# Performance work log

Measured on AMD Instinct MI355X. Metric: run time of the kernel, lower is better.

The kernel has to match this reference:

```python
import jax, jax.numpy as jnp
import numpy as np

N, D = 1024, 64  # n_nodes, inputSize == hiddenSize == cellSize


def setup_inputs() -> dict:
    key = jax.random.key(0)
    ks = jax.random.split(key, 9)
    inputs = jax.random.normal(ks[0], (N, D), dtype=jnp.float32)
    # sparse-ish binary adjacency, no self loops
    adj = (jax.random.uniform(ks[1], (N, N)) < 0.03).astype(jnp.float32)
    adj = adj.at[jnp.arange(N), jnp.arange(N)].set(0.0)
    numNei = jnp.maximum(adj.sum(axis=1), 1.0)  # avoid div-by-zero
    # initStates() in torch uses randn for h0/c0
    h0 = jax.random.normal(ks[2], (N, D), dtype=jnp.float32)
    c0 = jax.random.normal(ks[3], (N, D), dtype=jnp.float32)
    # torch nn.Linear default init: U(-1/sqrt(fan_in), 1/sqrt(fan_in))
    s_g = 1.0 / np.sqrt(2 * D)
    s_h = 1.0 / np.sqrt(D)
    Wg = jax.random.uniform(ks[4], (D, 2 * D), minval=-s_g, maxval=s_g, dtype=jnp.float32)
    bg = jax.random.uniform(ks[5], (D,), minval=-s_g, maxval=s_g, dtype=jnp.float32)
    Ws = jax.random.uniform(ks[6], (D, D), minval=-s_h, maxval=s_h, dtype=jnp.float32)
    bs = jax.random.uniform(ks[7], (D,), minval=-s_h, maxval=s_h, dtype=jnp.float32)
    Wn = jax.random.uniform(ks[8], (D, D), minval=-s_h, maxval=s_h, dtype=jnp.float32)
    sequence = jnp.arange(N, dtype=jnp.int32)
    return {"inputs": inputs, "neighbour": adj, "numNei": numNei,
            "h0": h0, "c0": c0, "Wg": Wg, "bg": bg, "Ws": Ws, "bs": bs,
            "Wn": Wn, "sequence": sequence}


def reference(inputs, neighbour, numNei, h0, c0, Wg, bg, Ws, bs, Wn, sequence):
    def step(carry, idx):
        H, C = carry                       # [N, D] each
        inp = inputs[idx]                  # [D]
        h_i = H[idx]                       # [D]
        c_i = C[idx]                       # [D] (torch passes cellState[index])
        nei = neighbour[idx]               # [N] adjacency row
        num = numNei[idx]
        # neighbour-averaged hidden state
        neiH = (nei @ H) / num             # [D]
        pre = jnp.concatenate([inp, h_i]) @ Wg.T + bg + neiH @ Wn.T  # [D]
        inputState = jax.nn.sigmoid(pre)
        outputState = inputState           # identical expression in torch
        helpCell = jnp.tanh(pre)
        fs = inp @ Ws.T + bs               # selfGate(inp), [D]
        # forgetSelfMat broadcast of fs over all nodes
        neiForget = jax.nn.sigmoid(fs[None, :] + H @ Wn.T)   # [N, D]
        forgetState = jax.nn.sigmoid(fs + h_i @ Wn.T)        # [D]
        c_new = (nei @ (neiForget * c_i[None, :])) / num \
                + forgetState * c_i + inputState * helpCell  # [D]
        h_new = jnp.tanh(outputState * c_new)
        return (H.at[idx].set(h_new), C.at[idx].set(c_new)), None

    (Hf, _Cf), _ = jax.lax.scan(step, (h0, c0), sequence)
    # torch: residualHidden aliases hiddenState and is mutated in-place,
    # so `hiddenState + residualHidden` == 2 * final hidden state.
    return Hf + Hf
```

## Files before the change

### kernel.cpp

```cpp
#include <hip/hip_runtime.h>

#define NN 1024
#define DD 64
#define CAP 96
#define RCAP 128
#define SENT 32768
#define NL2E -1.44269504088896f

typedef __attribute__((ext_vector_type(8))) short bf16x8;
typedef __attribute__((ext_vector_type(4))) float f32x4;

__device__ uint4    WnFragD[8*64];
__device__ float    FSd[NN*DD];
__device__ float    Gd[NN*DD];
__device__ float    preBaseD[NN*DD];
__device__ float    fpreD[NN*DD];
__device__ float4   nodeDatD[NN*DD];
__device__ int      lowNeiD[NN*CAP + 64];
__device__ int      revNeiD[NN*RCAP];
__device__ int      revCntD[NN];
__device__ int2     hdrD[NN];
__device__ int      posArr[NN];
__device__ float    invNumD[NN];

__device__ __forceinline__ float sigm(float x)  { return 1.0f / (1.0f + __expf(-x)); }
__device__ __forceinline__ float tanhf_(float x){ return 2.0f / (1.0f + __expf(-2.0f*x)) - 1.0f; }
__device__ __forceinline__ unsigned short bf16r(float x) {
  unsigned u = __float_as_uint(x);
  u = u + 0x7fffu + ((u >> 16) & 1u);
  return (unsigned short)(u >> 16);
}

__global__ __launch_bounds__(256) void k_node(const int* __restrict__ seq,
                                              const float* __restrict__ numNei,
                                              const float* __restrict__ inputs,
                                              const float* __restrict__ h0,
                                              const float* __restrict__ Wg,
                                              const float* __restrict__ bg,
                                              const float* __restrict__ Ws,
                                              const float* __restrict__ bs,
                                              const float* __restrict__ Wn) {
  __shared__ float x_l[4][64];
  __shared__ float hh_l[4][64];
  int tid = threadIdx.x;
  int gid = blockIdx.x * 256 + tid;
  if (gid < NN) { posArr[seq[gid]] = gid; invNumD[gid] = 1.0f / numNei[gid]; revCntD[gid] = 0; }
  if (gid < 512) {
    int st = gid >> 6, lane = gid & 63;
    int s = st >> 2, t = st & 3;
    int row = 16*t + (lane & 15);
    int k0 = 32*s + 8*(lane >> 4);
    const float* wr = &Wn[row*64 + k0];
    uint4 f;
    f.x = (unsigned)bf16r(wr[0]) | ((unsigned)bf16r(wr[1]) << 16);
    f.y = (unsigned)bf16r(wr[2]) | ((unsigned)bf16r(wr[3]) << 16);
    f.z = (unsigned)bf16r(wr[4]) | ((unsigned)bf16r(wr[5]) << 16);
    f.w = (unsigned)bf16r(wr[6]) | ((unsigned)bf16r(wr[7]) << 16);
    WnFragD[st*64 + lane] = f;
  }
  for (int e2 = gid; e2 < NN*CAP; e2 += 256*256) lowNeiD[e2] = SENT;
  int w = tid >> 6, d = tid & 63;
  int i = blockIdx.x * 4 + w;
  x_l[w][d]  = inputs[i*DD + d];
  hh_l[w][d] = h0[i*DD + d];
  __syncthreads();
  float afs = bs[d], apre = bg[d], ag0 = 0.0f;
  const float4* wsr = (const float4*)&Ws[d*64];
  const float4* wnr = (const float4*)&Wn[d*64];
  const float4* wga = (const float4*)&Wg[d*128];
  const float4* wgb = (const float4*)&Wg[d*128 + 64];
  #pragma unroll 4
  for (int k4 = 0; k4 < 16; ++k4) {
    float4 ws4 = wsr[k4], wn4 = wnr[k4], wa4 = wga[k4], wb4 = wgb[k4];
    const float* wsp = (const float*)&ws4;
    const float* wnp = (const float*)&wn4;
    const float* wap = (const float*)&wa4;
    const float* wbp = (const float*)&wb4;
    #pragma unroll
    for (int j = 0; j < 4; ++j) {
      int k = 4*k4 + j;
      float xk = x_l[w][k], hk = hh_l[w][k];
      afs  += xk * wsp[j];
      ag0  += hk * wnp[j];
      apre += xk * wap[j] + hk * wbp[j];
    }
  }
  FSd[i*DD + d]      = afs;
  Gd[i*DD + d]       = ag0;
  preBaseD[i*DD + d] = apre;
  fpreD[i*DD + d]    = sigm(afs + ag0);
}

__global__ __launch_bounds__(256) void k_edges(const float* __restrict__ adj,
                                               const float* __restrict__ c0) {
  int tid = threadIdx.x;
  int w = tid >> 6, d = tid & 63;
  int i = blockIdx.x * 4 + w;
  int pi = posArr[i];
  float fs = FSd[i*DD + d];
  float accP = 0.0f, accS = 0.0f;
  int cnt = 0;
  int myj = -1;
  for (int base = 0; base < NN; base += 64) {
    float a = adj[i*NN + base + d];
    unsigned long long mask = __ballot(a != 0.0f);
    while (mask) {
      int b = __ffsll(mask) - 1;
      mask &= (mask - 1);
      int j = base + b;
      if (posArr[j] < pi) {
        if (cnt == d) myj = j;
        cnt++;
      } else {
        float g = Gd[j*DD + d];
        accP += g;
        accS += sigm(fs + g);
      }
    }
  }
  int ccap = (cnt < 64) ? cnt : 64;
  if (d < ccap) {
    lowNeiD[i*CAP + d] = myj << 5;
    int slot = atomicAdd(&revCntD[myj], 1);
    if (slot < RCAP) revNeiD[myj*RCAP + slot] = i;
  }
  float inv = invNumD[i];
  if (d == 0) hdrD[i] = make_int2(ccap, __float_as_int(inv));
  float c0v = c0[i*DD + d];
  float civ = c0v * inv;
  nodeDatD[i*DD + d] = make_float4(NL2E * fs,
                                   preBaseD[i*DD + d] + accP * inv,
                                   civ,
                                   c0v * fpreD[i*DD + d] + civ * accS);
}

__global__ __launch_bounds__(1024, 4) void k_seq(float* __restrict__ out) {
  __shared__ unsigned long long Gl64[(NN*DD + 64)/4];
  __shared__ unsigned low8p[NN][4];
  __shared__ int      queue_[NN];
  __shared__ int      indeg[NN];
  __shared__ float    invL[NN];
  __shared__ unsigned short hstage[16][64];
  __shared__ int head, tail;
  unsigned short* Gl = (unsigned short*)Gl64;
  int tid  = threadIdx.x;
  int lane = tid & 63, w = tid >> 6;
  if (tid == 0) { head = 0; tail = 0; }
  queue_[tid] = -1;
  int2 hdr = hdrD[tid];
  int  rc  = revCntD[tid];
  int  cnt0 = hdr.x;
  indeg[tid] = cnt0 | (cnt0 << 8) | (rc << 15);
  invL[tid]  = __int_as_float(hdr.y);
  {
    uint4 a = *(const uint4*)&lowNeiD[tid*CAP];
    uint4 b = *(const uint4*)&lowNeiD[tid*CAP + 4];
    low8p[tid][0] = (a.x & 0xffffu) | (a.y << 16);
    low8p[tid][1] = (a.z & 0xffffu) | (a.w << 16);
    low8p[tid][2] = (b.x & 0xffffu) | (b.y << 16);
    low8p[tid][3] = (b.z & 0xffffu) | (b.w << 16);
  }
  if (tid < 16) Gl64[NN*DD/4 + tid] = 0ull;
  uint4 fb[2][4];
  #pragma unroll
  for (int s = 0; s < 2; ++s) {
    #pragma unroll
    for (int t = 0; t < 4; ++t)
      fb[s][t] = WnFragD[(s*4 + t)*64 + lane];
  }
  __syncthreads();
  if (cnt0 == 0) {
    int p = __hip_atomic_fetch_add(&tail, 1, __ATOMIC_RELAXED, __HIP_MEMORY_SCOPE_WORKGROUP);
    __hip_atomic_store(&queue_[p], tid | (rc << 17), __ATOMIC_RELEASE, __HIP_MEMORY_SCOPE_WORKGROUP);
  }
  __syncthreads();

  int t0 = 0;
  if (lane == 0) t0 = __hip_atomic_fetch_add(&head, 1, __ATOMIC_RELAXED, __HIP_MEMORY_SCOPE_WORKGROUP);
  int t = __builtin_amdgcn_readfirstlane(t0);
  int e = -1;
  if (t < NN) {
    e = __hip_atomic_load(&queue_[t], __ATOMIC_ACQUIRE, __HIP_MEMORY_SCOPE_WORKGROUP);
    while (e < 0)
      e = __hip_atomic_load(&queue_[t], __ATOMIC_ACQUIRE, __HIP_MEMORY_SCOPE_WORKGROUP);
  } else {
    return;
  }
  e = __builtin_amdgcn_readfirstlane(e);

  int    i, cnt, rcnt, jb2v, r0, r1;
  float4 nd;
  float  inv;
  uint4  lvv;
  #define ISSUE(E) do {                                               \
    i    = (E) & 1023;                                                \
    cnt  = ((E) >> 10) & 127;                                         \
    rcnt = ((E) >> 17) & 255;                                         \
    nd   = nodeDatD[i*DD + lane];                                     \
    jb2v = lowNeiD[i*CAP + 8 + lane];                                 \
    r0   = (lane < rcnt)      ? revNeiD[i*RCAP + lane]      : -1;     \
    r1   = (lane + 64 < rcnt) ? revNeiD[i*RCAP + 64 + lane] : -1;     \
    inv  = invL[i];                                                   \
    lvv  = *(uint4*)&low8p[i][0];                                     \
  } while (0)
  ISSUE(e);

  for (;;) {
    float fs2n = nd.x;
    float accG = 0.0f, accS = 0.0f;
    float g[32];
    #define LD(c) __uint_as_float(((unsigned)Gl[((c) << 1) + lane]) << 16)
    if (cnt > 0) {
      g[0]=LD(lvv.x & 0xffffu); g[1]=LD(lvv.x >> 16);
      g[2]=LD(lvv.y & 0xffffu); g[3]=LD(lvv.y >> 16);
    }
    if (cnt > 4) {
      g[4]=LD(lvv.z & 0xffffu); g[5]=LD(lvv.z >> 16);
      g[6]=LD(lvv.w & 0xffffu); g[7]=LD(lvv.w >> 16);
    }
    if (cnt > 8) {
      #pragma unroll
      for (int q = 0; q < 4; ++q) g[8+q]  = LD(__builtin_amdgcn_readlane(jb2v, q));
    }
    if (cnt > 12) {
      #pragma unroll
      for (int q = 0; q < 4; ++q) g[12+q] = LD(__builtin_amdgcn_readlane(jb2v, 4+q));
    }
    if (cnt > 16) {
      #pragma unroll
      for (int q = 0; q < 4; ++q) g[16+q] = LD(__builtin_amdgcn_readlane(jb2v, 8+q));
    }
    if (cnt > 20) {
      #pragma unroll
      for (int q = 0; q < 4; ++q) g[20+q] = LD(__builtin_amdgcn_readlane(jb2v, 12+q));
    }
    if (cnt > 24) {
      #pragma unroll
      for (int q = 0; q < 4; ++q) g[24+q] = LD(__builtin_amdgcn_readlane(jb2v, 16+q));
    }
    if (cnt > 28) {
      #pragma unroll
      for (int q = 0; q < 4; ++q) g[28+q] = LD(__builtin_amdgcn_readlane(jb2v, 20+q));
    }
    auto quad = [&](float ga, float gb, float gc, float gd) {
      float xa = fminf(__builtin_fmaf(ga, NL2E, fs2n), 25.0f);
      float xb = fminf(__builtin_fmaf(gb, NL2E, fs2n), 25.0f);
      float xc = fminf(__builtin_fmaf(gc, NL2E, fs2n), 25.0f);
      float xd = fminf(__builtin_fmaf(gd, NL2E, fs2n), 25.0f);
      float ea = __builtin_amdgcn_exp2f(xa);
      float eb = __builtin_amdgcn_exp2f(xb);
      float ec = __builtin_amdgcn_exp2f(xc);
      float ed = __builtin_amdgcn_exp2f(xd);
      float s0 = ea + eb, n0 = s0 + 2.0f;
      float d0 = __builtin_fmaf(ea, eb, s0) + 1.0f;
      float s1 = ec + ed, n1 = s1 + 2.0f;
      float d1 = __builtin_fmaf(ec, ed, s1) + 1.0f;
      float Nn = __builtin_fmaf(n0, d1, n1 * d0);
      float Dd = d0 * d1;
      accS = __builtin_fmaf(Nn, __builtin_amdgcn_rcpf(Dd), accS);
      accG += (ga + gb) + (gc + gd);
    };
    if (cnt > 0)  quad(g[0],  g[1],  g[2],  g[3]);
    if (cnt > 4)  quad(g[4],  g[5],  g[6],  g[7]);
    if (cnt > 8)  quad(g[8],  g[9],  g[10], g[11]);
    if (cnt > 12) quad(g[12], g[13], g[14], g[15]);
    if (cnt > 16) quad(g[16], g[17], g[18], g[19]);
    if (cnt > 20) quad(g[20], g[21], g[22], g[23]);
    if (cnt > 24) quad(g[24], g[25], g[26], g[27]);
    if (cnt > 28) quad(g[28], g[29], g[30], g[31]);
    if (cnt > 32) {
      for (int base = 32; base < cnt; base += 4) {
        float ga = LD(__builtin_amdgcn_readlane(jb2v, base - 8));
        float gb = LD(__builtin_amdgcn_readlane(jb2v, base - 7));
        float gc = LD(__builtin_amdgcn_readlane(jb2v, base - 6));
        float gd = LD(__builtin_amdgcn_readlane(jb2v, base - 5));
        quad(ga, gb, gc, gd);
      }
    }
    {
      int slots = (cnt <= 32) ? ((cnt + 3) & ~3) : (32 + ((cnt - 32 + 3) & ~3));
      float e0   = __builtin_amdgcn_exp2f(fminf(fs2n, 25.0f));
      float sig0 = __builtin_amdgcn_rcpf(1.0f + e0);
      accS -= (float)(slots - cnt) * sig0;
    }
    float pre = nd.y + inv * accG;
    float is  = sigm(pre);
    float hcl = tanhf_(pre);
    float c   = nd.z * accS + nd.w + is * hcl;
    float h   = tanhf_(is * c);
    int ic = i, r0c = r0, r1c = r1;
    if (lane == 0) t0 = __hip_atomic_fetch_add(&head, 1, __ATOMIC_RELAXED, __HIP_MEMORY_SCOPE_WORKGROUP);
    t = __builtin_amdgcn_readfirstlane(t0);
    bool done = (t >= NN);
    int e2 = -1;
    if (!done) e2 = __hip_atomic_load(&queue_[t], __ATOMIC_ACQUIRE, __HIP_MEMORY_SCOPE_WORKGROUP);
    e2 = __builtin_amdgcn_readfirstlane(e2);
    bool pre_ok = (e2 >= 0);
    if (pre_ok) ISSUE(e2);
    hstage[w][lane] = bf16r(h);
    const uint4* hv = (const uint4*)&hstage[w][0];
    uint4 fa0 = hv[lane >> 4];
    uint4 fa1 = hv[4 + (lane >> 4)];
    f32x4 z = {0.f, 0.f, 0.f, 0.f};
    f32x4 a0 = __builtin_amdgcn_mfma_f32_16x16x32_bf16(__builtin_bit_cast(bf16x8, fa0), __builtin_bit_cast(bf16x8, fb[0][0]), z, 0, 0, 0);
    f32x4 a1 = __builtin_amdgcn_mfma_f32_16x16x32_bf16(__builtin_bit_cast(bf16x8, fa0), __builtin_bit_cast(bf16x8, fb[0][1]), z, 0, 0, 0);
    f32x4 a2 = __builtin_amdgcn_mfma_f32_16x16x32_bf16(__builtin_bit_cast(bf16x8, fa0), __builtin_bit_cast(bf16x8, fb[0][2]), z, 0, 0, 0);
    f32x4 a3 = __builtin_amdgcn_mfma_f32_16x16x32_bf16(__builtin_bit_cast(bf16x8, fa0), __builtin_bit_cast(bf16x8, fb[0][3]), z, 0, 0, 0);
    a0 = __builtin_amdgcn_mfma_f32_16x16x32_bf16(__builtin_bit_cast(bf16x8, fa1), __builtin_bit_cast(bf16x8, fb[1][0]), a0, 0, 0, 0);
    a1 = __builtin_amdgcn_mfma_f32_16x16x32_bf16(__builtin_bit_cast(bf16x8, fa1), __builtin_bit_cast(bf16x8, fb[1][1]), a1, 0, 0, 0);
    a2 = __builtin_amdgcn_mfma_f32_16x16x32_bf16(__builtin_bit_cast(bf16x8, fa1), __builtin_bit_cast(bf16x8, fb[1][2]), a2, 0, 0, 0);
    a3 = __builtin_amdgcn_mfma_f32_16x16x32_bf16(__builtin_bit_cast(bf16x8, fa1), __builtin_bit_cast(bf16x8, fb[1][3]), a3, 0, 0, 0);
    float r01 = (lane & 16) ? a1[0] : a0[0];
    float r23 = (lane & 16) ? a3[0] : a2[0];
    float rg  = (lane & 32) ? r23 : r01;
    Gl[(ic << 6) + lane] = bf16r(rg);
    if (r0c >= 0) {
      int old = __hip_atomic_fetch_add(&indeg[r0c], -1, __ATOMIC_ACQ_REL, __HIP_MEMORY_SCOPE_WORKGROUP);
      if ((old & 0xff) == 1) {
        int p = __hip_atomic_fetch_add(&tail, 1, __ATOMIC_RELAXED, __HIP_MEMORY_SCOPE_WORKGROUP);
        int en = r0c | (((old >> 8) & 127) << 10) | (((old >> 15) & 255) << 17);
        __hip_atomic_store(&queue_[p], en, __ATOMIC_RELEASE, __HIP_MEMORY_SCOPE_WORKGROUP);
      }
    }
    if (r1c >= 0) {
      int old = __hip_atomic_fetch_add(&indeg[r1c], -1, __ATOMIC_ACQ_REL, __HIP_MEMORY_SCOPE_WORKGROUP);
      if ((old & 0xff) == 1) {
        int p = __hip_atomic_fetch_add(&tail, 1, __ATOMIC_RELAXED, __HIP_MEMORY_SCOPE_WORKGROUP);
        int en = r1c | (((old >> 8) & 127) << 10) | (((old >> 15) & 255) << 17);
        __hip_atomic_store(&queue_[p], en, __ATOMIC_RELEASE, __HIP_MEMORY_SCOPE_WORKGROUP);
      }
    }
    out[ic*DD + lane] = 2.0f * h;
    if (done) break;
    if (!pre_ok) {
      int e3 = __hip_atomic_load(&queue_[t], __ATOMIC_ACQUIRE, __HIP_MEMORY_SCOPE_WORKGROUP);
      while (e3 < 0)
        e3 = __hip_atomic_load(&queue_[t], __ATOMIC_ACQUIRE, __HIP_MEMORY_SCOPE_WORKGROUP);
      e3 = __builtin_amdgcn_readfirstlane(e3);
      ISSUE(e3);
    }
  }
  #undef LD
  #undef ISSUE
}

extern "C" void kernel_launch(void* const* d_in, const int* in_sizes, int n_in,
                              void* d_out, int out_size, void* d_ws, size_t ws_size,
                              hipStream_t stream) {
  const float* inputs = (const float*)d_in[0];
  const float* adj    = (const float*)d_in[1];
  const float* numNei = (const float*)d_in[2];
  const float* h0     = (const float*)d_in[3];
  const float* c0     = (const float*)d_in[4];
  const float* Wg     = (const float*)d_in[5];
  const float* bg     = (const float*)d_in[6];
  const float* Ws     = (const float*)d_in[7];
  const float* bs     = (const float*)d_in[8];
  const float* Wn     = (const float*)d_in[9];
  const int*   seq    = (const int*)d_in[10];
  float* out = (float*)d_out;

  k_node <<<256, 256, 0, stream>>>(seq, numNei, inputs, h0, Wg, bg, Ws, bs, Wn);
  k_edges<<<256, 256, 0, stream>>>(adj, c0);
  k_seq  <<<1, 1024, 0, stream>>>(out);
}
```

Baseline: 191.7 us.

## Keep a newly-readied successor node in the same wave instead of enqueueing it

After finishing a node, each wave now gathers the successors that just became ready. It keeps one of them to process itself and pushes only the others onto the shared queue. This is meant to save the queue round-trip (tail atomic, store, head atomic, load) on the critical dependency chain and to give cache-friendly continuation. Because a wave may now exit the queue early, a doneCnt counter is added so idle waves waiting on an empty slot can terminate. The cost is that the next item is no longer prefetched before the MFMA/store phase, and waiters must poll an extra shared counter.

```diff
diff --git a/kernel.cpp b/kernel.cpp
--- a/kernel.cpp
+++ b/kernel.cpp
@@ -141,11 +141,11 @@
   __shared__ int      indeg[NN];
   __shared__ float    invL[NN];
   __shared__ unsigned short hstage[16][64];
-  __shared__ int head, tail;
+  __shared__ int head, tail, doneCnt;
   unsigned short* Gl = (unsigned short*)Gl64;
   int tid  = threadIdx.x;
   int lane = tid & 63, w = tid >> 6;
-  if (tid == 0) { head = 0; tail = 0; }
+  if (tid == 0) { head = 0; tail = 0; doneCnt = 0; }
   queue_[tid] = -1;
   int2 hdr = hdrD[tid];
   int  rc  = revCntD[tid];
@@ -289,14 +289,6 @@
     float c   = nd.z * accS + nd.w + is * hcl;
     float h   = tanhf_(is * c);
     int ic = i, r0c = r0, r1c = r1;
-    if (lane == 0) t0 = __hip_atomic_fetch_add(&head, 1, __ATOMIC_RELAXED, __HIP_MEMORY_SCOPE_WORKGROUP);
-    t = __builtin_amdgcn_readfirstlane(t0);
-    bool done = (t >= NN);
-    int e2 = -1;
-    if (!done) e2 = __hip_atomic_load(&queue_[t], __ATOMIC_ACQUIRE, __HIP_MEMORY_SCOPE_WORKGROUP);
-    e2 = __builtin_amdgcn_readfirstlane(e2);
-    bool pre_ok = (e2 >= 0);
-    if (pre_ok) ISSUE(e2);
     hstage[w][lane] = bf16r(h);
     const uint4* hv = (const uint4*)&hstage[w][0];
     uint4 fa0 = hv[lane >> 4];
@@ -314,31 +306,55 @@
     float r23 = (lane & 16) ? a3[0] : a2[0];
     float rg  = (lane & 32) ? r23 : r01;
     Gl[(ic << 6) + lane] = bf16r(rg);
+    int en0 = -1, en1 = -1;
     if (r0c >= 0) {
       int old = __hip_atomic_fetch_add(&indeg[r0c], -1, __ATOMIC_ACQ_REL, __HIP_MEMORY_SCOPE_WORKGROUP);
-      if ((old & 0xff) == 1) {
-        int p = __hip_atomic_fetch_add(&tail, 1, __ATOMIC_RELAXED, __HIP_MEMORY_SCOPE_WORKGROUP);
-        int en = r0c | (((old >> 8) & 127) << 10) | (((old >> 15) & 255) << 17);
-        __hip_atomic_store(&queue_[p], en, __ATOMIC_RELEASE, __HIP_MEMORY_SCOPE_WORKGROUP);
-      }
+      if ((old & 0xff) == 1)
+        en0 = r0c | (((old >> 8) & 127) << 10) | (((old >> 15) & 255) << 17);
     }
     if (r1c >= 0) {
       int old = __hip_atomic_fetch_add(&indeg[r1c], -1, __ATOMIC_ACQ_REL, __HIP_MEMORY_SCOPE_WORKGROUP);
-      if ((old & 0xff) == 1) {
-        int p = __hip_atomic_fetch_add(&tail, 1, __ATOMIC_RELAXED, __HIP_MEMORY_SCOPE_WORKGROUP);
-        int en = r1c | (((old >> 8) & 127) << 10) | (((old >> 15) & 255) << 17);
-        __hip_atomic_store(&queue_[p], en, __ATOMIC_RELEASE, __HIP_MEMORY_SCOPE_WORKGROUP);
-      }
+      if ((old & 0xff) == 1)
+        en1 = r1c | (((old >> 8) & 127) << 10) | (((old >> 15) & 255) << 17);
+    }
+    unsigned long long m0 = __ballot(en0 >= 0);
+    unsigned long long m1 = __ballot(en1 >= 0);
+    int keepEn = -1, kl = -1, ks = -1;
+    if (m0) {
+      kl = __ffsll(m0) - 1; ks = 0;
+      keepEn = __builtin_amdgcn_readlane(en0, kl);
+    } else if (m1) {
+      kl = __ffsll(m1) - 1; ks = 1;
+      keepEn = __builtin_amdgcn_readlane(en1, kl);
+    }
+    if (en0 >= 0 && !(ks == 0 && lane == kl)) {
+      int p = __hip_atomic_fetch_add(&tail, 1, __ATOMIC_RELAXED, __HIP_MEMORY_SCOPE_WORKGROUP);
+      __hip_atomic_store(&queue_[p], en0, __ATOMIC_RELEASE, __HIP_MEMORY_SCOPE_WORKGROUP);
+    }
+    if (en1 >= 0 && !(ks == 1 && lane == kl)) {
+      int p = __hip_atomic_fetch_add(&tail, 1, __ATOMIC_RELAXED, __HIP_MEMORY_SCOPE_WORKGROUP);
+      __hip_atomic_store(&queue_[p], en1, __ATOMIC_RELEASE, __HIP_MEMORY_SCOPE_WORKGROUP);
+    }
+    if (lane == 0)
+      __hip_atomic_fetch_add(&doneCnt, 1, __ATOMIC_RELAXED, __HIP_MEMORY_SCOPE_WORKGROUP);
+    if (keepEn >= 0) {
+      ISSUE(keepEn);
+      out[ic*DD + lane] = 2.0f * h;
+      continue;
     }
     out[ic*DD + lane] = 2.0f * h;
-    if (done) break;
-    if (!pre_ok) {
-      int e3 = __hip_atomic_load(&queue_[t], __ATOMIC_ACQUIRE, __HIP_MEMORY_SCOPE_WORKGROUP);
-      while (e3 < 0)
-        e3 = __hip_atomic_load(&queue_[t], __ATOMIC_ACQUIRE, __HIP_MEMORY_SCOPE_WORKGROUP);
-      e3 = __builtin_amdgcn_readfirstlane(e3);
-      ISSUE(e3);
-    }
+    if (lane == 0) t0 = __hip_atomic_fetch_add(&head, 1, __ATOMIC_RELAXED, __HIP_MEMORY_SCOPE_WORKGROUP);
+    t = __builtin_amdgcn_readfirstlane(t0);
+    if (t >= NN) break;
+    int e3;
+    for (;;) {
+      e3 = __hip_atomic_load(&queue_[t], __ATOMIC_ACQUIRE, __HIP_MEMORY_SCOPE_WORKGROUP);
+      if (e3 >= 0) break;
+      if (__hip_atomic_load(&doneCnt, __ATOMIC_RELAXED, __HIP_MEMORY_SCOPE_WORKGROUP) == NN) break;
+    }
+    if (e3 < 0) break;
+    e3 = __builtin_amdgcn_readfirstlane(e3);
+    ISSUE(e3);
   }
   #undef LD
   #undef ISSUE
```

Result: faster. 181.8 us (median of 2 runs) (-5.2%).
